# Optimization experiments

Measured on AMD Instinct MI355X. Metric: run time of the kernel, lower is better.

## Reference

```python
import jax, jax.numpy as jnp
import numpy as np


def setup_inputs() -> dict:
    key = jax.random.key(0)
    k_adj, k_ann, k_b = jax.random.split(key, 3)
    B, N, F = 8, 4096, 64
    # Adjacency: sparse-ish nonnegative matrix (TF version stores it as tf.sparse;
    raw = jax.random.uniform(k_adj, (B, N, N), dtype=jnp.float32)
    adjacent = jnp.where(raw > 0.95, raw, 0.0)
    annotations = jax.random.normal(k_ann, (B, N, F), dtype=jnp.float32)
    bias = jax.random.normal(k_b, (1, 1, F), dtype=jnp.float32)
    return {"adjacent": adjacent, "annotations": annotations, "bias": bias}


def reference(adjacent, annotations, bias):
    # Per-batch sparse @ dense matmul in TF == batched matmul here.
    # adjacent: [B,N,N], annotations: [B,N,F] -> [B,N,F]
    out = jnp.einsum('bnm,bmf->bnf', adjacent, annotations)
    return out + bias
```

## Files before the change

### kernel.cpp

```cpp
#include <hip/hip_runtime.h>
#include <stdint.h>

typedef __bf16 bf16x8 __attribute__((ext_vector_type(8)));
typedef float f32x16 __attribute__((ext_vector_type(16)));

#define NN 4096
#define FF 64
#define BM 64
#define BK 64
#define NSTEP (NN / BK)

__device__ __forceinline__ unsigned short f2bf(float x) {
    unsigned int u = __builtin_bit_cast(unsigned int, x);
    unsigned int r = u + 0x7fffu + ((u >> 16) & 1u);
    return (unsigned short)(r >> 16);
}

__device__ __forceinline__ void gload16(const void* g, void* l) {
    __builtin_amdgcn_global_load_lds((const __attribute__((address_space(1))) void*)g,
                                     (__attribute__((address_space(3))) void*)l, 16, 0, 0);
}

__global__ __launch_bounds__(256) void annT_kernel(const float* __restrict__ ann,
                                                   unsigned short* __restrict__ annT) {
    __shared__ unsigned short tile[FF * 66];
    int b = blockIdx.x >> 6;
    int m0 = (blockIdx.x & 63) << 6;
    int t = threadIdx.x;
    int f = t & 63;
    int ml = t >> 6;
    const float* src = ann + ((size_t)(b * NN + m0)) * FF;
#pragma unroll
    for (int it = 0; it < 16; ++it) {
        int m = it * 4 + ml;
        tile[f * 66 + m] = f2bf(src[(size_t)m * FF + f]);
    }
    __syncthreads();
    int m2 = (t & 31) * 2;
    int fr = t >> 5;
    unsigned short* dst = annT + (size_t)b * FF * NN + m0;
#pragma unroll
    for (int it = 0; it < 8; ++it) {
        int fo = it * 8 + fr;
        unsigned int lo = tile[fo * 66 + m2];
        unsigned int hi = tile[fo * 66 + m2 + 1];
        *(unsigned int*)(dst + (size_t)fo * NN + m2) = lo | (hi << 16);
    }
}

__global__ __launch_bounds__(256, 2) void gconv_kernel(const float* __restrict__ A,
                                                       const unsigned short* __restrict__ annT,
                                                       const float* __restrict__ bias,
                                                       float* __restrict__ out) {
    __shared__ alignas(16) char lds[2][24576];

    int bi = blockIdx.x;
    int b = bi & 7;
    int n0 = (bi >> 3) << 6;
    int t = threadIdx.x, lane = t & 63, wid = t >> 6;
    int wm = wid >> 1, wf = wid & 1;
    int r = lane & 31, h = lane >> 5;

    const float* Ab = A + (size_t)b * NN * NN + (size_t)n0 * NN;
    const unsigned short* Tb = annT + (size_t)b * FF * NN;

    const float* asrc[4];
#pragma unroll
    for (int j = 0; j < 4; ++j) {
        unsigned s = (unsigned)(wid * 4096 + j * 1024 + lane * 16);
        unsigned row = s >> 8;
        unsigned q = ((s & 255u) ^ ((row & 15u) << 4)) >> 4;
        asrc[j] = Ab + (size_t)row * NN + q * 4;
    }
    const unsigned short* bsrc[2];
#pragma unroll
    for (int j = 0; j < 2; ++j) {
        unsigned s = (unsigned)(wid * 2048 + j * 1024 + lane * 16);
        unsigned f = s >> 7;
        unsigned q = ((s & 127u) ^ ((f & 7u) << 4)) >> 4;
        bsrc[j] = Tb + (size_t)f * NN + q * 8;
    }

    auto STAGE = [&](int buf, int k0) {
        char* base = lds[buf];
#pragma unroll
        for (int j = 0; j < 4; ++j)
            gload16(asrc[j] + k0, base + wid * 4096 + j * 1024);
#pragma unroll
        for (int j = 0; j < 2; ++j)
            gload16(bsrc[j] + k0, base + 16384 + wid * 2048 + j * 1024);
    };

    int arow = wm * 32 + r;
    unsigned abase = (unsigned)(arow * 256);
    unsigned aswz = (unsigned)((arow & 15) << 4);
    int frow = wf * 32 + r;
    unsigned bbase = (unsigned)(frow * 128);
    unsigned bswz = (unsigned)((frow & 7) << 4);

    f32x16 acc = {};

    STAGE(0, 0);
#pragma unroll 1
    for (int s = 0; s < NSTEP; ++s) {
        int cur = s & 1;
        if (s + 1 < NSTEP) {
            STAGE(cur ^ 1, (s + 1) * BK);
            asm volatile("s_waitcnt vmcnt(6)" ::: "memory");
        } else {
            asm volatile("s_waitcnt vmcnt(0)" ::: "memory");
        }
        __builtin_amdgcn_s_barrier();
        asm volatile("" ::: "memory");

        const char* bufA = lds[cur];
        const char* bufB = lds[cur] + 16384;
#pragma unroll
        for (int kc = 0; kc < 4; ++kc) {
            unsigned ao = abase + (unsigned)(kc * 64 + h * 32);
            float4 a0 = *(const float4*)(bufA + ((ao) ^ aswz));
            float4 a1 = *(const float4*)(bufA + ((ao + 16) ^ aswz));
            bf16x8 af = {(__bf16)a0.x, (__bf16)a0.y, (__bf16)a0.z, (__bf16)a0.w,
                         (__bf16)a1.x, (__bf16)a1.y, (__bf16)a1.z, (__bf16)a1.w};
            unsigned bo = (bbase + (unsigned)(kc * 32 + h * 16)) ^ bswz;
            bf16x8 bf = *(const bf16x8*)(bufB + bo);
            acc = __builtin_amdgcn_mfma_f32_32x32x16_bf16(af, bf, acc, 0, 0, 0);
        }
        asm volatile("" ::: "memory");
        __builtin_amdgcn_s_barrier();
        asm volatile("" ::: "memory");
    }

    float bv = bias[wf * 32 + r];
    float* ob = out + ((size_t)(b * NN + n0 + wm * 32)) * FF + wf * 32 + r;
#pragma unroll
    for (int e = 0; e < 16; ++e) {
        int rowl = (e & 3) + 8 * (e >> 2) + h * 4;
        ob[(size_t)rowl * FF] = acc[e] + bv;
    }
}

extern "C" void kernel_launch(void* const* d_in, const int* in_sizes, int n_in,
                              void* d_out, int out_size, void* d_ws, size_t ws_size,
                              hipStream_t stream) {
    const float* adj = (const float*)d_in[0];
    const float* ann = (const float*)d_in[1];
    const float* bias = (const float*)d_in[2];
    float* out = (float*)d_out;
    unsigned short* annT = (unsigned short*)d_ws;

    annT_kernel<<<dim3(8 * (NN / 64)), dim3(256), 0, stream>>>(ann, annT);
    gconv_kernel<<<dim3(8 * (NN / BM)), dim3(256), 0, stream>>>(adj, annT, bias, out);
}
```

Baseline: 707.3 us.

## Pre-pack annotations into MFMA fragment layout and load B directly to registers

The preprocessing kernel now writes annotations as bf16 in a layout that matches the per-lane MFMA B-fragment order, replacing the transposed layout. The main kernel loads B fragments straight from global/L2 into registers each step instead of staging them through LDS, which shrinks LDS per buffer and drops the B-side LDS reads. The vmcnt waits are adjusted to account for the extra outstanding register loads. In exchange, B loads are no longer shared across waves through LDS, so each wave fetches its own B data from cache. The register loads are also issued right before they are used, with less latency hiding than before.

```diff
diff --git a/kernel.cpp b/kernel.cpp
--- a/kernel.cpp
+++ b/kernel.cpp
@@ -9,6 +9,7 @@
 #define BM 64
 #define BK 64
 #define NSTEP (NN / BK)
+#define NKB (NN / 16)
 
 __device__ __forceinline__ unsigned short f2bf(float x) {
     unsigned int u = __builtin_bit_cast(unsigned int, x);
@@ -21,38 +22,29 @@
                                      (__attribute__((address_space(3))) void*)l, 16, 0, 0);
 }
 
-__global__ __launch_bounds__(256) void annT_kernel(const float* __restrict__ ann,
-                                                   unsigned short* __restrict__ annT) {
-    __shared__ unsigned short tile[FF * 66];
-    int b = blockIdx.x >> 6;
-    int m0 = (blockIdx.x & 63) << 6;
-    int t = threadIdx.x;
-    int f = t & 63;
-    int ml = t >> 6;
-    const float* src = ann + ((size_t)(b * NN + m0)) * FF;
+__global__ __launch_bounds__(256) void annP_kernel(const float* __restrict__ ann,
+                                                   unsigned short* __restrict__ annP) {
+    int blk = blockIdx.x;
+    int b = blk >> 6;
+    int kb = (blk & 63) * 4 + (threadIdx.x >> 6);
+    int f = threadIdx.x & 63;
+    const float* src = ann + (size_t)(b * NN + kb * 16) * FF + f;
+    unsigned short v[16];
 #pragma unroll
-    for (int it = 0; it < 16; ++it) {
-        int m = it * 4 + ml;
-        tile[f * 66 + m] = f2bf(src[(size_t)m * FF + f]);
-    }
-    __syncthreads();
-    int m2 = (t & 31) * 2;
-    int fr = t >> 5;
-    unsigned short* dst = annT + (size_t)b * FF * NN + m0;
+    for (int kh = 0; kh < 16; ++kh) v[kh] = f2bf(src[(size_t)kh * FF]);
+    unsigned int p[8];
 #pragma unroll
-    for (int it = 0; it < 8; ++it) {
-        int fo = it * 8 + fr;
-        unsigned int lo = tile[fo * 66 + m2];
-        unsigned int hi = tile[fo * 66 + m2 + 1];
-        *(unsigned int*)(dst + (size_t)fo * NN + m2) = lo | (hi << 16);
-    }
+    for (int i = 0; i < 8; ++i) p[i] = (unsigned)v[2 * i] | ((unsigned)v[2 * i + 1] << 16);
+    uint4* dst = (uint4*)(annP + ((size_t)(b * NKB + kb) * 64 + f) * 16);
+    dst[0] = make_uint4(p[0], p[1], p[2], p[3]);
+    dst[1] = make_uint4(p[4], p[5], p[6], p[7]);
 }
 
 __global__ __launch_bounds__(256, 2) void gconv_kernel(const float* __restrict__ A,
-                                                       const unsigned short* __restrict__ annT,
+                                                       const unsigned short* __restrict__ annP,
                                                        const float* __restrict__ bias,
                                                        float* __restrict__ out) {
-    __shared__ alignas(16) char lds[2][24576];
+    __shared__ alignas(16) char lds[2][16384];
 
     int bi = blockIdx.x;
     int b = bi & 7;
@@ -62,7 +54,6 @@
     int r = lane & 31, h = lane >> 5;
 
     const float* Ab = A + (size_t)b * NN * NN + (size_t)n0 * NN;
-    const unsigned short* Tb = annT + (size_t)b * FF * NN;
 
     const float* asrc[4];
 #pragma unroll
@@ -72,59 +63,48 @@
         unsigned q = ((s & 255u) ^ ((row & 15u) << 4)) >> 4;
         asrc[j] = Ab + (size_t)row * NN + q * 4;
     }
-    const unsigned short* bsrc[2];
-#pragma unroll
-    for (int j = 0; j < 2; ++j) {
-        unsigned s = (unsigned)(wid * 2048 + j * 1024 + lane * 16);
-        unsigned f = s >> 7;
-        unsigned q = ((s & 127u) ^ ((f & 7u) << 4)) >> 4;
-        bsrc[j] = Tb + (size_t)f * NN + q * 8;
-    }
-
     auto STAGE = [&](int buf, int k0) {
         char* base = lds[buf];
 #pragma unroll
-        for (int j = 0; j < 4; ++j)
-            gload16(asrc[j] + k0, base + wid * 4096 + j * 1024);
-#pragma unroll
-        for (int j = 0; j < 2; ++j)
-            gload16(bsrc[j] + k0, base + 16384 + wid * 2048 + j * 1024);
+        for (int j = 0; j < 4; ++j) gload16(asrc[j] + k0, base + wid * 4096 + j * 1024);
     };
 
-    int arow = wm * 32 + r;
-    unsigned abase = (unsigned)(arow * 256);
-    unsigned aswz = (unsigned)((arow & 15) << 4);
-    int frow = wf * 32 + r;
-    unsigned bbase = (unsigned)(frow * 128);
-    unsigned bswz = (unsigned)((frow & 7) << 4);
+    const unsigned short* bfp =
+        annP + (size_t)b * NKB * 64 * 16 + (size_t)(wf * 32 + r) * 16 + h * 8;
+
+    unsigned abase = (unsigned)((wm * 32 + r) * 256);
+    unsigned aswz = (unsigned)(((wm * 32 + r) & 15) << 4);
 
     f32x16 acc = {};
+    uint4 bfrag[4];
 
     STAGE(0, 0);
 #pragma unroll 1
     for (int s = 0; s < NSTEP; ++s) {
         int cur = s & 1;
+        int kb0 = s * 4;
+#pragma unroll
+        for (int kc = 0; kc < 4; ++kc)
+            bfrag[kc] = *(const uint4*)(bfp + (size_t)(kb0 + kc) * 1024);
         if (s + 1 < NSTEP) {
             STAGE(cur ^ 1, (s + 1) * BK);
-            asm volatile("s_waitcnt vmcnt(6)" ::: "memory");
+            asm volatile("s_waitcnt vmcnt(8)" ::: "memory");
         } else {
-            asm volatile("s_waitcnt vmcnt(0)" ::: "memory");
+            asm volatile("s_waitcnt vmcnt(4)" ::: "memory");
         }
         __builtin_amdgcn_s_barrier();
         asm volatile("" ::: "memory");
 
         const char* bufA = lds[cur];
-        const char* bufB = lds[cur] + 16384;
 #pragma unroll
         for (int kc = 0; kc < 4; ++kc) {
             unsigned ao = abase + (unsigned)(kc * 64 + h * 32);
-            float4 a0 = *(const float4*)(bufA + ((ao) ^ aswz));
+            float4 a0 = *(const float4*)(bufA + (ao ^ aswz));
             float4 a1 = *(const float4*)(bufA + ((ao + 16) ^ aswz));
             bf16x8 af = {(__bf16)a0.x, (__bf16)a0.y, (__bf16)a0.z, (__bf16)a0.w,
                          (__bf16)a1.x, (__bf16)a1.y, (__bf16)a1.z, (__bf16)a1.w};
-            unsigned bo = (bbase + (unsigned)(kc * 32 + h * 16)) ^ bswz;
-            bf16x8 bf = *(const bf16x8*)(bufB + bo);
-            acc = __builtin_amdgcn_mfma_f32_32x32x16_bf16(af, bf, acc, 0, 0, 0);
+            acc = __builtin_amdgcn_mfma_f32_32x32x16_bf16(
+                af, __builtin_bit_cast(bf16x8, bfrag[kc]), acc, 0, 0, 0);
         }
         asm volatile("" ::: "memory");
         __builtin_amdgcn_s_barrier();
@@ -147,8 +127,8 @@
     const float* ann = (const float*)d_in[1];
     const float* bias = (const float*)d_in[2];
     float* out = (float*)d_out;
-    unsigned short* annT = (unsigned short*)d_ws;
+    unsigned short* annP = (unsigned short*)d_ws;
 
-    annT_kernel<<<dim3(8 * (NN / 64)), dim3(256), 0, stream>>>(ann, annT);
-    gconv_kernel<<<dim3(8 * (NN / BM)), dim3(256), 0, stream>>>(adj, annT, bias, out);
+    annP_kernel<<<dim3(8 * 64), dim3(256), 0, stream>>>(ann, annP);
+    gconv_kernel<<<dim3(8 * (NN / BM)), dim3(256), 0, stream>>>(adj, annP, bias, out);
 }
```

New measurement: 707.7 us. No clear change (+0.1%).
